# Optimization experiments

Measured on AMD Instinct MI355X. Metric: run time of the kernel, lower is better.

Reference implementation:

```python
import jax, jax.numpy as jnp
import numpy as np

NUM_EMBEDDINGS = 16384
EMBEDDING_DIM = 512
COMMITMENT_COST = 0.25  # legacy: vq_loss = commit + beta * codebook
NORM_EPS = 1e-12  # F.normalize default eps


def setup_inputs() -> dict:
    key = jax.random.key(0)
    k_z, k_emb, k_w, k_b = jax.random.split(key, 4)
    z = jax.random.normal(k_z, (8, 1024, EMBEDDING_DIM), dtype=jnp.float32)
    # frozen codebook, init normal with std = D^{-0.5}
    embedding_weight = jax.random.normal(k_emb, (NUM_EMBEDDINGS, EMBEDDING_DIM), dtype=jnp.float32) * (EMBEDDING_DIM ** -0.5)
    # learnable projection (torch Linear: y = x @ W.T + b, W is [out, in])
    bound = 1.0 / np.sqrt(EMBEDDING_DIM)
    proj_w = jax.random.uniform(k_w, (EMBEDDING_DIM, EMBEDDING_DIM), dtype=jnp.float32, minval=-bound, maxval=bound)
    proj_b = jax.random.uniform(k_b, (EMBEDDING_DIM,), dtype=jnp.float32, minval=-bound, maxval=bound)
    scale = jnp.asarray(10.0, dtype=jnp.float32)
    return {"z": z, "embedding_weight": embedding_weight, "proj_w": proj_w, "proj_b": proj_b, "scale": scale}


def _l2_normalize(x):
    n = jnp.linalg.norm(x, axis=-1, keepdims=True)
    return x / jnp.maximum(n, NORM_EPS)


def reference(z, embedding_weight, proj_w, proj_b, scale):
    B, N, D = z.shape
    z_flat = z.reshape(-1, D)                                   # [M, D]
    quant_codebook = embedding_weight @ proj_w.T + proj_b       # [K, D]
    z_n = _l2_normalize(z_flat)
    c_n = _l2_normalize(quant_codebook)
    distances = -(z_n @ c_n.T) * scale                          # [M, K]
    encoding_indices = jnp.argmin(distances, axis=1)            # [M]
    quantized = quant_codebook[encoding_indices].reshape(z.shape)
    commitment_loss = jnp.mean((jax.lax.stop_gradient(quantized) - z) ** 2)
    codebook_loss = jnp.mean((quantized - jax.lax.stop_gradient(z)) ** 2)
    vq_loss = commitment_loss + COMMITMENT_COST * codebook_loss  # legacy=True
    quantized = z + jax.lax.stop_gradient(quantized - z)         # straight-through
    encoding_indices = encoding_indices.reshape(B, N)
    return quantized, vq_loss, encoding_indices
```

## Files before the change

### kernel.cpp

```cpp
#include <hip/hip_runtime.h>
#include <math.h>


typedef _Float16 f16;
typedef _Float16 f16x8 __attribute__((ext_vector_type(8)));
typedef _Float16 f16x4 __attribute__((ext_vector_type(4)));
typedef short s16x8 __attribute__((ext_vector_type(8)));
typedef float f32x4 __attribute__((ext_vector_type(4)));
typedef unsigned int u32;
typedef unsigned long long u64;
typedef unsigned short ushort_t;

#define INV2048 (1.0f/2048.0f)
#define MARGIN  0.010f

#define OFF_Q    0u
#define OFF_EHI  33554432u
#define OFF_ELO  50331648u
#define OFF_WHI  67108864u
#define OFF_WLO  67633152u
#define OFF_CB   68157440u
#define OFF_ZB   84934656u
#define OFF_RL   93323264u
#define OFF_PK   OFF_EHI

__device__ __forceinline__ void gload_lds16(const void* g, void* l) {
  __builtin_amdgcn_global_load_lds(
      (const __attribute__((address_space(1))) u32*)g,
      (__attribute__((address_space(3))) u32*)l, 16, 0, 0);
}

__device__ __forceinline__ void stage_tile(const void* __restrict__ src, int row0,
                                           int kt, char* lds, int tid) {
#pragma unroll
  for (int i = 0; i < 4; ++i) {
    int lin = i * 256 + tid;
    int row = lin >> 3;
    int slot = lin & 7;
    int k8 = slot ^ (row & 7);
    const char* g = (const char*)src + (((size_t)(row0 + row)) << 10)
                    + (size_t)(kt * 128 + k8 * 16);
    gload_lds16(g, lds + lin * 16);
  }
}

__device__ __forceinline__ u64 make_key(float v, int idx) {
  u32 b = __float_as_uint(v);
  u32 m = (u32)((int)b >> 31) | 0x80000000u;
  return ((u64)(b ^ m) << 32) | (u32)(0x7FFFFFFF - idx);
}
__device__ __forceinline__ float key_val(u64 k) {
  u32 o = (u32)(k >> 32);
  u32 m = (o & 0x80000000u) ? 0x80000000u : 0xFFFFFFFFu;
  return __uint_as_float(o ^ m);
}
__device__ __forceinline__ int key_idx(u64 k) {
  return 0x7FFFFFFF - (int)(u32)(k & 0xFFFFFFFFu);
}
__device__ __forceinline__ u64 umax64(u64 a, u64 b) { return a > b ? a : b; }

#define LDS_AHI 0
#define LDS_ALO 16384
#define LDS_BHI 32768
#define LDS_BLO 49152

__global__ __launch_bounds__(256, 2) void k_gemm_codebook(
    const f16* __restrict__ Ahi, const f16* __restrict__ Alo,
    const f16* __restrict__ Bhi, const f16* __restrict__ Blo,
    const float* __restrict__ bias, float* __restrict__ Q) {
  __shared__ __align__(16) char lds[65536];
  f32x4 hh[4][4], xx[4][4];
  const int tid = threadIdx.x;
  const int m0 = blockIdx.y * 128;
  const int n0 = blockIdx.x * 128;
  const int l = tid & 63;
  const int wid = tid >> 6;
  const int wr = (wid >> 1) * 64;
  const int wc = (wid & 1) * 64;
  const int r7 = (l & 15) & 7;

#pragma unroll
  for (int a = 0; a < 4; ++a)
#pragma unroll
    for (int b = 0; b < 4; ++b) {
      hh[a][b] = (f32x4){0.f, 0.f, 0.f, 0.f};
      xx[a][b] = (f32x4){0.f, 0.f, 0.f, 0.f};
    }

  for (int kt = 0; kt < 8; ++kt) {
    stage_tile(Ahi, m0, kt, lds + LDS_AHI, tid);
    stage_tile(Alo, m0, kt, lds + LDS_ALO, tid);
    stage_tile(Bhi, n0, kt, lds + LDS_BHI, tid);
    stage_tile(Blo, n0, kt, lds + LDS_BLO, tid);
    __syncthreads();
#pragma unroll
    for (int ks = 0; ks < 2; ++ks) {
      const int kg = ks * 4 + (l >> 4);
      const int s = (kg ^ r7) * 16;
      const char* pa = lds + (wr + (l & 15)) * 128 + s;
      const char* pb = lds + (wc + (l & 15)) * 128 + s;
      f16x8 ahi[4], alo[4];
#pragma unroll
      for (int mf = 0; mf < 4; ++mf) {
        ahi[mf] = *(const f16x8*)(pa + LDS_AHI + mf * 2048);
        alo[mf] = *(const f16x8*)(pa + LDS_ALO + mf * 2048);
      }
#pragma unroll
      for (int nf = 0; nf < 4; ++nf) {
        f16x8 bhi = *(const f16x8*)(pb + LDS_BHI + nf * 2048);
        f16x8 blo = *(const f16x8*)(pb + LDS_BLO + nf * 2048);
#pragma unroll
        for (int mf = 0; mf < 4; ++mf) {
          hh[mf][nf] = __builtin_amdgcn_mfma_f32_16x16x32_f16(ahi[mf], bhi, hh[mf][nf], 0, 0, 0);
          xx[mf][nf] = __builtin_amdgcn_mfma_f32_16x16x32_f16(ahi[mf], blo, xx[mf][nf], 0, 0, 0);
          xx[mf][nf] = __builtin_amdgcn_mfma_f32_16x16x32_f16(alo[mf], bhi, xx[mf][nf], 0, 0, 0);
        }
      }
    }
    __syncthreads();
  }

#pragma unroll
  for (int mf = 0; mf < 4; ++mf)
#pragma unroll
    for (int nf = 0; nf < 4; ++nf)
#pragma unroll
      for (int j = 0; j < 4; ++j) {
        int row = m0 + wr + mf * 16 + (l >> 4) * 4 + j;
        int col = n0 + wc + nf * 16 + (l & 15);
        Q[(size_t)row * 512 + col] = hh[mf][nf][j] + xx[mf][nf][j] * INV2048 + bias[col];
      }
}

__global__ __launch_bounds__(256, 4) void k_gemm_coarse(
    const ushort_t* __restrict__ CB, const ushort_t* __restrict__ ZB,
    u64* __restrict__ pk) {
  __shared__ __align__(16) char lds[32768];
  f32x4 acc[4][4];
  const int tid = threadIdx.x;
  const int cb0 = blockIdx.x * 128;
  const int zb0 = blockIdx.y * 128;
  const int l = tid & 63;
  const int wid = tid >> 6;
  const int wr = (wid >> 1);
  const int wc = (wid & 1);

  const int rA0 = tid >> 2, sA0 = tid & 3;
  const int rA1 = (tid + 256) >> 2, sA1 = tid & 3;
  const u32 ga0 = (u32)(rA0 * 1024 + ((sA0 ^ (rA0 & 3)) * 16));
  const u32 ga1 = (u32)(rA1 * 1024 + ((sA1 ^ (rA1 & 3)) * 16));
  const char* gA = (const char*)CB + ((size_t)cb0 << 10);
  const char* gB = (const char*)ZB + ((size_t)zb0 << 10);
  const u32 d0 = (u32)tid * 16;
  const u32 d1 = d0 + 4096;

#define STAGE32(KT, BUF)                                                       \
  {                                                                            \
    char* db_ = lds + (BUF) * 16384;                                           \
    const u32 ko_ = (u32)(KT) * 64;                                            \
    gload_lds16(gA + ga0 + ko_, db_ + d0);                                     \
    gload_lds16(gA + ga1 + ko_, db_ + d1);                                     \
    gload_lds16(gB + ga0 + ko_, db_ + 8192 + d0);                              \
    gload_lds16(gB + ga1 + ko_, db_ + 8192 + d1);                              \
  }

  const u32 sphys = (u32)((((l >> 4)) ^ ((l & 15) & 3)) * 16);
  const u32 aoff = (u32)((wr * 64 + (l & 15)) * 64) + sphys;
  const u32 boff = 8192u + (u32)((wc * 64 + (l & 15)) * 64) + sphys;

#pragma unroll
  for (int a = 0; a < 4; ++a)
#pragma unroll
    for (int b = 0; b < 4; ++b) acc[a][b] = (f32x4){0.f, 0.f, 0.f, 0.f};

#define COMPUTE32(BUF)                                                         \
  {                                                                            \
    const char* base_ = lds + (BUF) * 16384;                                   \
    s16x8 af[4];                                                               \
    _Pragma("unroll") for (int mf = 0; mf < 4; ++mf)                           \
      af[mf] = *(const s16x8*)(base_ + aoff + mf * 1024);                      \
    _Pragma("unroll") for (int nf = 0; nf < 4; ++nf) {                         \
      s16x8 bf = *(const s16x8*)(base_ + boff + nf * 1024);                    \
      _Pragma("unroll") for (int mf = 0; mf < 4; ++mf)                         \
        acc[mf][nf] = __builtin_amdgcn_mfma_f32_16x16x32_bf16(af[mf], bf, acc[mf][nf], 0, 0, 0); \
    }                                                                          \
  }

  STAGE32(0, 0)
  __syncthreads();
#pragma unroll 2
  for (int kt = 0; kt < 15; ++kt) {
    STAGE32(kt + 1, (kt & 1) ^ 1)
    COMPUTE32(kt & 1)
    __syncthreads();
  }
  COMPUTE32(1)
  __syncthreads();

  float* cmax = (float*)lds;
  u32* cnt = (u32*)(lds + 1024);
  u64* slots = (u64*)(lds + 2048);

  float cm[4];
#pragma unroll
  for (int nf = 0; nf < 4; ++nf) {
    float m = acc[0][nf][0];
#pragma unroll
    for (int mf = 0; mf < 4; ++mf)
#pragma unroll
      for (int j = 0; j < 4; ++j) m = fmaxf(m, acc[mf][nf][j]);
    m = fmaxf(m, __shfl_xor(m, 16, 64));
    m = fmaxf(m, __shfl_xor(m, 32, 64));
    cm[nf] = m;
  }
  if (tid < 128) cnt[tid] = 0;
  slots[tid] = 0;
  slots[tid + 256] = 0;
  if ((l >> 4) == 0) {
#pragma unroll
    for (int nf = 0; nf < 4; ++nf)
      cmax[(wc * 64 + nf * 16 + l) * 2 + wr] = cm[nf];
  }
  __syncthreads();

#pragma unroll
  for (int nf = 0; nf < 4; ++nf) {
    int col = wc * 64 + nf * 16 + (l & 15);
    float thresh = fmaxf(cmax[col * 2], cmax[col * 2 + 1]) - MARGIN;
#pragma unroll
    for (int mf = 0; mf < 4; ++mf)
#pragma unroll
      for (int j = 0; j < 4; ++j) {
        float v = acc[mf][nf][j];
        if (v >= thresh) {
          int code = cb0 + wr * 64 + mf * 16 + ((l >> 4) << 2) + j;
          u32 p = atomicAdd(&cnt[col], 1u);
          if (p < 4) slots[col * 4 + p] = make_key(v, code);
        }
      }
  }
  __syncthreads();

  if (tid < 128) {
    size_t base = (((size_t)(zb0 + tid)) * 128 + blockIdx.x) * 4;
#pragma unroll
    for (int s = 0; s < 4; ++s) pk[base + s] = slots[tid * 4 + s];
  }
#undef STAGE32
#undef COMPUTE32
}

__global__ __launch_bounds__(256) void k_split(const float* __restrict__ src,
                                               f16* __restrict__ hi,
                                               f16* __restrict__ lo, int n4) {
  int i = blockIdx.x * 256 + threadIdx.x;
  if (i >= n4) return;
  const float4 v = ((const float4*)src)[i];
  f16 h0 = (f16)v.x, h1 = (f16)v.y, h2 = (f16)v.z, h3 = (f16)v.w;
  ((f16x4*)hi)[i] = (f16x4){h0, h1, h2, h3};
  ((f16x4*)lo)[i] = (f16x4){(f16)((v.x - (float)h0) * 2048.0f),
                            (f16)((v.y - (float)h1) * 2048.0f),
                            (f16)((v.z - (float)h2) * 2048.0f),
                            (f16)((v.w - (float)h3) * 2048.0f)};
}

__device__ __forceinline__ ushort_t f2bf_rne(float f) {
  u32 b = __float_as_uint(f);
  b += 0x7FFFu + ((b >> 16) & 1u);
  return (ushort_t)(b >> 16);
}

__global__ __launch_bounds__(256) void k_norm_bf16(const float* __restrict__ src,
                                                   ushort_t* __restrict__ dst) {
  __shared__ float red[256];
  const int row = blockIdx.x, t = threadIdx.x;
  float q0 = src[(size_t)row * 512 + t];
  float q1 = src[(size_t)row * 512 + t + 256];
  red[t] = q0 * q0 + q1 * q1;
  __syncthreads();
  for (int s = 128; s > 0; s >>= 1) {
    if (t < s) red[t] += red[t + s];
    __syncthreads();
  }
  float inv = 1.0f / fmaxf(sqrtf(red[0]), 1e-12f);
  dst[(size_t)row * 512 + t] = f2bf_rne(q0 * inv);
  dst[(size_t)row * 512 + t + 256] = f2bf_rne(q1 * inv);
}

__global__ __launch_bounds__(256) void k_rescore_gather(
    const u64* __restrict__ pk, const float* __restrict__ Q,
    const float* __restrict__ z, float* __restrict__ outq,
    float* __restrict__ outidx, float* __restrict__ rloss) {
  __shared__ float sz[512];
  __shared__ double redd[8];
  __shared__ u64 redk[4];
  __shared__ int cand[64];
  __shared__ int ccount;
  const int row = blockIdx.x, t = threadIdx.x;

  sz[t] = z[(size_t)row * 512 + t];
  sz[t + 256] = z[(size_t)row * 512 + t + 256];
  if (t == 0) ccount = 0;

  u64 k1 = pk[(size_t)row * 512 + t * 2];
  u64 k2 = pk[(size_t)row * 512 + t * 2 + 1];
  u64 km = umax64(k1, k2);
  for (int m = 1; m < 64; m <<= 1)
    km = umax64(km, (u64)__shfl_xor((long long)km, m));
  if ((t & 63) == 0) redk[t >> 6] = km;
  __syncthreads();
  u64 gk = umax64(umax64(redk[0], redk[1]), umax64(redk[2], redk[3]));
  float thresh = key_val(gk) - MARGIN;

  if (key_val(k1) >= thresh) { int p = atomicAdd(&ccount, 1); if (p < 64) cand[p] = key_idx(k1); }
  if (key_val(k2) >= thresh) { int p = atomicAdd(&ccount, 1); if (p < 64) cand[p] = key_idx(k2); }
  __syncthreads();
  int nc = ccount < 64 ? ccount : 64;

  double bs = -1e300;
  int bi = 0x7FFFFFFF;
  for (int c = 0; c < nc; ++c) {
    int code = cand[c];
    const float* Qr = Q + (size_t)code * 512;
    double dotp = 0.0, qq = 0.0;
#pragma unroll
    for (int h = 0; h < 2; ++h) {
      int d = t + h * 256;
      double qv = (double)Qr[d];
      dotp += (double)sz[d] * qv;
      qq += qv * qv;
    }
    for (int m = 1; m < 64; m <<= 1) {
      dotp += __shfl_xor(dotp, m);
      qq += __shfl_xor(qq, m);
    }
    if ((t & 63) == 0) { redd[t >> 6] = dotp; redd[4 + (t >> 6)] = qq; }
    __syncthreads();
    double dsum = redd[0] + redd[1] + redd[2] + redd[3];
    double qsum = redd[4] + redd[5] + redd[6] + redd[7];
    double s = dsum / fmax(sqrt(qsum), 1e-12);
    if (s > bs || (s == bs && code < bi)) { bs = s; bi = code; }
    __syncthreads();
  }

  const float* Qb = Q + (size_t)bi * 512;
  double lsum = 0.0;
#pragma unroll
  for (int h = 0; h < 2; ++h) {
    int d = t + h * 256;
    float qv = Qb[d], zv = sz[d];
    outq[(size_t)row * 512 + d] = zv + (qv - zv);
    float df = qv - zv;
    lsum += (double)df * (double)df;
  }
  for (int m = 1; m < 64; m <<= 1) lsum += __shfl_xor(lsum, m);
  if ((t & 63) == 0) redd[t >> 6] = lsum;
  __syncthreads();
  if (t == 0) {
    rloss[row] = (float)(redd[0] + redd[1] + redd[2] + redd[3]);
    outidx[row] = (float)bi;
  }
}

__global__ __launch_bounds__(256) void k_loss_final(const float* __restrict__ rloss,
                                                    float* __restrict__ out_loss) {
  __shared__ float sl[256];
  int t = threadIdx.x;
  float s = 0.f;
#pragma unroll
  for (int i = 0; i < 32; ++i) s += rloss[t + i * 256];
  sl[t] = s;
  __syncthreads();
  for (int k = 128; k > 0; k >>= 1) {
    if (t < k) sl[t] += sl[t + k];
    __syncthreads();
  }
  if (t == 0) out_loss[0] = 1.25f * sl[0] / 4194304.0f;
}

extern "C" void kernel_launch(void* const* d_in, const int* in_sizes, int n_in,
                              void* d_out, int out_size, void* d_ws, size_t ws_size,
                              hipStream_t stream) {
  const float* z = (const float*)d_in[0];
  const float* emb = (const float*)d_in[1];
  const float* pw = (const float*)d_in[2];
  const float* pb = (const float*)d_in[3];

  char* ws = (char*)d_ws;
  float* Q = (float*)(ws + OFF_Q);
  f16* ehi = (f16*)(ws + OFF_EHI);
  f16* elo = (f16*)(ws + OFF_ELO);
  f16* whi = (f16*)(ws + OFF_WHI);
  f16* wlo = (f16*)(ws + OFF_WLO);
  ushort_t* cb = (ushort_t*)(ws + OFF_CB);
  ushort_t* zb = (ushort_t*)(ws + OFF_ZB);
  u64* pk = (u64*)(ws + OFF_PK);
  float* rloss = (float*)(ws + OFF_RL);

  float* outq = (float*)d_out;
  float* outloss = outq + 4194304;
  float* outidx = outq + 4194305;

  k_split<<<8192, 256, 0, stream>>>(emb, ehi, elo, 2097152);
  k_split<<<256, 256, 0, stream>>>(pw, whi, wlo, 65536);
  k_norm_bf16<<<8192, 256, 0, stream>>>(z, zb);
  k_gemm_codebook<<<dim3(4, 128), 256, 0, stream>>>(ehi, elo, whi, wlo, pb, Q);
  k_norm_bf16<<<16384, 256, 0, stream>>>(Q, cb);
  k_gemm_coarse<<<dim3(128, 64), 256, 0, stream>>>(cb, zb, pk);
  k_rescore_gather<<<8192, 256, 0, stream>>>(pk, Q, z, outq, outidx, rloss);
  k_loss_final<<<1, 256, 0, stream>>>(rloss, outloss);
}
```

Measured before the change: 307.6 us.

## Fuse preprocessing kernels, read codebook B operand from global, fix LDS swizzle

Merges the two split launches and the z normalization into a single k_pre kernel, removing two launches and their gaps. In the codebook GEMM, the projection-weight (B) fragments are now loaded straight from global memory instead of staged through LDS, which halves LDS use and may raise occupancy at the cost of uncoalesced per-fragment global reads. The coarse GEMM's LDS swizzle changes from row&3 to (row>>2)&3 to reduce bank conflicts on fragment reads.

Result: slower. 320.2 us (+4.1%).

```diff
diff --git a/kernel.cpp b/kernel.cpp
--- a/kernel.cpp
+++ b/kernel.cpp
@@ -59,16 +59,52 @@
 }
 __device__ __forceinline__ u64 umax64(u64 a, u64 b) { return a > b ? a : b; }
 
-#define LDS_AHI 0
-#define LDS_ALO 16384
-#define LDS_BHI 32768
-#define LDS_BLO 49152
+__device__ __forceinline__ ushort_t f2bf_rne(float f) {
+  u32 b = __float_as_uint(f);
+  b += 0x7FFFu + ((b >> 16) & 1u);
+  return (ushort_t)(b >> 16);
+}
+
+__global__ __launch_bounds__(256) void k_pre(
+    const float* __restrict__ emb, const float* __restrict__ pw,
+    const float* __restrict__ z, f16* __restrict__ ehi, f16* __restrict__ elo,
+    f16* __restrict__ whi, f16* __restrict__ wlo, ushort_t* __restrict__ zb) {
+  __shared__ float red[256];
+  const int bid = blockIdx.x, t = threadIdx.x;
+  if (bid < 8448) {
+    const float* src;
+    f16 *hi, *lo;
+    int i;
+    if (bid < 8192) { src = emb; hi = ehi; lo = elo; i = bid * 256 + t; }
+    else            { src = pw;  hi = whi; lo = wlo; i = (bid - 8192) * 256 + t; }
+    const float4 v = ((const float4*)src)[i];
+    f16 h0 = (f16)v.x, h1 = (f16)v.y, h2 = (f16)v.z, h3 = (f16)v.w;
+    ((f16x4*)hi)[i] = (f16x4){h0, h1, h2, h3};
+    ((f16x4*)lo)[i] = (f16x4){(f16)((v.x - (float)h0) * 2048.0f),
+                              (f16)((v.y - (float)h1) * 2048.0f),
+                              (f16)((v.z - (float)h2) * 2048.0f),
+                              (f16)((v.w - (float)h3) * 2048.0f)};
+  } else {
+    const int row = bid - 8448;
+    float q0 = z[(size_t)row * 512 + t];
+    float q1 = z[(size_t)row * 512 + t + 256];
+    red[t] = q0 * q0 + q1 * q1;
+    __syncthreads();
+    for (int s = 128; s > 0; s >>= 1) {
+      if (t < s) red[t] += red[t + s];
+      __syncthreads();
+    }
+    float inv = 1.0f / fmaxf(sqrtf(red[0]), 1e-12f);
+    zb[(size_t)row * 512 + t] = f2bf_rne(q0 * inv);
+    zb[(size_t)row * 512 + t + 256] = f2bf_rne(q1 * inv);
+  }
+}
 
 __global__ __launch_bounds__(256, 2) void k_gemm_codebook(
     const f16* __restrict__ Ahi, const f16* __restrict__ Alo,
     const f16* __restrict__ Bhi, const f16* __restrict__ Blo,
     const float* __restrict__ bias, float* __restrict__ Q) {
-  __shared__ __align__(16) char lds[65536];
+  __shared__ __align__(16) char lds[32768];
   f32x4 hh[4][4], xx[4][4];
   const int tid = threadIdx.x;
   const int m0 = blockIdx.y * 128;
@@ -79,6 +115,11 @@
   const int wc = (wid & 1) * 64;
   const int r7 = (l & 15) & 7;
 
+  const size_t brow = (size_t)(n0 + wc + (l & 15)) << 10;
+  const u32 bko = (u32)((l >> 4) * 16);
+  const char* gBhi = (const char*)Bhi + brow + bko;
+  const char* gBlo = (const char*)Blo + brow + bko;
+
 #pragma unroll
   for (int a = 0; a < 4; ++a)
 #pragma unroll
@@ -88,27 +129,25 @@
     }
 
   for (int kt = 0; kt < 8; ++kt) {
-    stage_tile(Ahi, m0, kt, lds + LDS_AHI, tid);
-    stage_tile(Alo, m0, kt, lds + LDS_ALO, tid);
-    stage_tile(Bhi, n0, kt, lds + LDS_BHI, tid);
-    stage_tile(Blo, n0, kt, lds + LDS_BLO, tid);
+    stage_tile(Ahi, m0, kt, lds, tid);
+    stage_tile(Alo, m0, kt, lds + 16384, tid);
     __syncthreads();
 #pragma unroll
     for (int ks = 0; ks < 2; ++ks) {
       const int kg = ks * 4 + (l >> 4);
       const int s = (kg ^ r7) * 16;
       const char* pa = lds + (wr + (l & 15)) * 128 + s;
-      const char* pb = lds + (wc + (l & 15)) * 128 + s;
       f16x8 ahi[4], alo[4];
 #pragma unroll
       for (int mf = 0; mf < 4; ++mf) {
-        ahi[mf] = *(const f16x8*)(pa + LDS_AHI + mf * 2048);
-        alo[mf] = *(const f16x8*)(pa + LDS_ALO + mf * 2048);
+        ahi[mf] = *(const f16x8*)(pa + mf * 2048);
+        alo[mf] = *(const f16x8*)(pa + 16384 + mf * 2048);
       }
+      const u32 bk = (u32)(kt * 128 + ks * 64);
 #pragma unroll
       for (int nf = 0; nf < 4; ++nf) {
-        f16x8 bhi = *(const f16x8*)(pb + LDS_BHI + nf * 2048);
-        f16x8 blo = *(const f16x8*)(pb + LDS_BLO + nf * 2048);
+        f16x8 bhi = *(const f16x8*)(gBhi + nf * 16384 + bk);
+        f16x8 blo = *(const f16x8*)(gBlo + nf * 16384 + bk);
 #pragma unroll
         for (int mf = 0; mf < 4; ++mf) {
           hh[mf][nf] = __builtin_amdgcn_mfma_f32_16x16x32_f16(ahi[mf], bhi, hh[mf][nf], 0, 0, 0);
@@ -146,9 +185,9 @@
   const int wc = (wid & 1);
 
   const int rA0 = tid >> 2, sA0 = tid & 3;
-  const int rA1 = (tid + 256) >> 2, sA1 = tid & 3;
-  const u32 ga0 = (u32)(rA0 * 1024 + ((sA0 ^ (rA0 & 3)) * 16));
-  const u32 ga1 = (u32)(rA1 * 1024 + ((sA1 ^ (rA1 & 3)) * 16));
+  const int rA1 = (tid + 256) >> 2;
+  const u32 ga0 = (u32)(rA0 * 1024 + ((sA0 ^ ((rA0 >> 2) & 3)) * 16));
+  const u32 ga1 = (u32)(rA1 * 1024 + ((sA0 ^ ((rA1 >> 2) & 3)) * 16));
   const char* gA = (const char*)CB + ((size_t)cb0 << 10);
   const char* gB = (const char*)ZB + ((size_t)zb0 << 10);
   const u32 d0 = (u32)tid * 16;
@@ -164,7 +203,7 @@
     gload_lds16(gB + ga1 + ko_, db_ + 8192 + d1);                              \
   }
 
-  const u32 sphys = (u32)((((l >> 4)) ^ ((l & 15) & 3)) * 16);
+  const u32 sphys = (u32)((((l >> 4)) ^ (((l & 15) >> 2) & 3)) * 16);
   const u32 aoff = (u32)((wr * 64 + (l & 15)) * 64) + sphys;
   const u32 boff = 8192u + (u32)((wc * 64 + (l & 15)) * 64) + sphys;
 
@@ -250,26 +289,6 @@
 #undef COMPUTE32
 }
 
-__global__ __launch_bounds__(256) void k_split(const float* __restrict__ src,
-                                               f16* __restrict__ hi,
-                                               f16* __restrict__ lo, int n4) {
-  int i = blockIdx.x * 256 + threadIdx.x;
-  if (i >= n4) return;
-  const float4 v = ((const float4*)src)[i];
-  f16 h0 = (f16)v.x, h1 = (f16)v.y, h2 = (f16)v.z, h3 = (f16)v.w;
-  ((f16x4*)hi)[i] = (f16x4){h0, h1, h2, h3};
-  ((f16x4*)lo)[i] = (f16x4){(f16)((v.x - (float)h0) * 2048.0f),
-                            (f16)((v.y - (float)h1) * 2048.0f),
-                            (f16)((v.z - (float)h2) * 2048.0f),
-                            (f16)((v.w - (float)h3) * 2048.0f)};
-}
-
-__device__ __forceinline__ ushort_t f2bf_rne(float f) {
-  u32 b = __float_as_uint(f);
-  b += 0x7FFFu + ((b >> 16) & 1u);
-  return (ushort_t)(b >> 16);
-}
-
 __global__ __launch_bounds__(256) void k_norm_bf16(const float* __restrict__ src,
                                                    ushort_t* __restrict__ dst) {
   __shared__ float red[256];
@@ -401,9 +420,7 @@
   float* outloss = outq + 4194304;
   float* outidx = outq + 4194305;
 
-  k_split<<<8192, 256, 0, stream>>>(emb, ehi, elo, 2097152);
-  k_split<<<256, 256, 0, stream>>>(pw, whi, wlo, 65536);
-  k_norm_bf16<<<8192, 256, 0, stream>>>(z, zb);
+  k_pre<<<16640, 256, 0, stream>>>(emb, pw, z, ehi, elo, whi, wlo, zb);
   k_gemm_codebook<<<dim3(4, 128), 256, 0, stream>>>(ehi, elo, whi, wlo, pb, Q);
   k_norm_bf16<<<16384, 256, 0, stream>>>(Q, cb);
   k_gemm_coarse<<<dim3(128, 64), 256, 0, stream>>>(cb, zb, pk);
```
